# Kernel optimization log

Hardware: AMD Instinct MI355X
Metric: run time of the kernel (lower is better)

## Reference

```python
import jax, jax.numpy as jnp
import numpy as np

N, D, E = 50000, 128, 800000
BN_EPS = 1e-3  # keras BatchNormalization default


def _ffn_block(x, g, b, m, v, W, bias):
    # BatchNorm (inference) -> Dropout (identity at inference) -> Dense + exact GELU
    xn = (x - m) * g * jax.lax.rsqrt(v + BN_EPS) + b
    return jax.nn.gelu(xn @ W + bias, approximate=False)


def setup_inputs() -> dict:
    key = jax.random.key(0)
    ks = jax.random.split(key, 24)
    inp = {
        "node_reps": jax.random.normal(ks[0], (N, D), dtype=jnp.float32),
        "edges": jax.random.randint(ks[1], (2, E), 0, N, dtype=jnp.int32),
        "edge_weights": jax.random.uniform(ks[2], (E,), dtype=jnp.float32),
    }
    def bn(i, dim):
        return (jax.random.normal(ks[i], (dim,)) * 0.1 + 1.0,   # gamma
                jax.random.normal(ks[i + 1], (dim,)) * 0.1,      # beta
                jax.random.normal(ks[i + 2], (dim,)) * 0.1,      # moving mean
                jax.random.uniform(ks[i + 3], (dim,)) + 0.5)     # moving var (>0)
    # prepare FFN: two blocks, D->D then D->D
    inp["pre_bn1_g"], inp["pre_bn1_b"], inp["pre_bn1_m"], inp["pre_bn1_v"] = bn(3, D)
    inp["pre_w1"] = jax.random.normal(ks[7], (D, D)) * (1.0 / np.sqrt(D))
    inp["pre_b1"] = jnp.zeros((D,), jnp.float32)
    inp["pre_bn2_g"], inp["pre_bn2_b"], inp["pre_bn2_m"], inp["pre_bn2_v"] = bn(8, D)
    inp["pre_w2"] = jax.random.normal(ks[12], (D, D)) * (1.0 / np.sqrt(D))
    inp["pre_b2"] = jnp.zeros((D,), jnp.float32)
    # update FFN: concat -> 2D input, then D->D
    inp["upd_bn1_g"], inp["upd_bn1_b"], inp["upd_bn1_m"], inp["upd_bn1_v"] = bn(13, 2 * D)
    inp["upd_w1"] = jax.random.normal(ks[17], (2 * D, D)) * (1.0 / np.sqrt(2 * D))
    inp["upd_b1"] = jnp.zeros((D,), jnp.float32)
    inp["upd_bn2_g"], inp["upd_bn2_b"], inp["upd_bn2_m"], inp["upd_bn2_v"] = bn(18, D)
    inp["upd_w2"] = jax.random.normal(ks[22], (D, D)) * (1.0 / np.sqrt(D))
    inp["upd_b2"] = jnp.zeros((D,), jnp.float32)
    return inp


def reference(node_reps, edges, edge_weights,
              pre_bn1_g, pre_bn1_b, pre_bn1_m, pre_bn1_v, pre_w1, pre_b1,
              pre_bn2_g, pre_bn2_b, pre_bn2_m, pre_bn2_v, pre_w2, pre_b2,
              upd_bn1_g, upd_bn1_b, upd_bn1_m, upd_bn1_v, upd_w1, upd_b1,
              upd_bn2_g, upd_bn2_b, upd_bn2_m, upd_bn2_v, upd_w2, upd_b2):
    num_nodes = node_reps.shape[0]
    node_idx, nbr_idx = edges[0], edges[1]
    # gather neighbour representations [E, D]
    nbr = jnp.take(node_reps, nbr_idx, axis=0)
    # prepare: FFN then scale by edge weights
    msg = _ffn_block(nbr, pre_bn1_g, pre_bn1_b, pre_bn1_m, pre_bn1_v, pre_w1, pre_b1)
    msg = _ffn_block(msg, pre_bn2_g, pre_bn2_b, pre_bn2_m, pre_bn2_v, pre_w2, pre_b2)
    msg = msg * edge_weights[:, None]
    # aggregate: segment_sum scatter back to nodes [N, D]
    agg = jax.ops.segment_sum(msg, node_idx, num_segments=num_nodes)
    # update: concat + FFN, then L2 normalize
    h = jnp.concatenate([node_reps, agg], axis=-1)  # [N, 2D]
    out = _ffn_block(h, upd_bn1_g, upd_bn1_b, upd_bn1_m, upd_bn1_v, upd_w1, upd_b1)
    out = _ffn_block(out, upd_bn2_g, upd_bn2_b, upd_bn2_m, upd_bn2_v, upd_w2, upd_b2)
    out = out * jax.lax.rsqrt(jnp.maximum(jnp.sum(out * out, axis=-1, keepdims=True), 1e-12))
    return out
```

## Files before the change

### kernel.cpp

```cpp
#include <hip/hip_runtime.h>
#include <hip/hip_bf16.h>
#include <math.h>

#define NN 50000
#define DD 128
#define EE 800000

static constexpr float BN_EPS = 1e-3f;

typedef __attribute__((ext_vector_type(8))) short bf16x8;
typedef __attribute__((ext_vector_type(4))) float f32x4;

#define MFMA16(a, b, c) __builtin_amdgcn_mfma_f32_16x16x32_bf16((a), (b), (c), 0, 0, 0)

__device__ __forceinline__ float gelu_f(float x) {
    float ax = fabsf(x) * 0.7071067811865475f;
    float t = __builtin_amdgcn_rcpf(fmaf(0.3275911f, ax, 1.0f));
    float p = t * fmaf(t, fmaf(t, fmaf(t, fmaf(t, 1.061405429f, -1.453152027f),
                                       1.421413741f), -0.284496736f), 0.254829592f);
    float e = __expf(-ax * ax);
    float er = fmaf(-p, e, 1.0f);
    float s = copysignf(er, x);
    return 0.5f * x * (1.0f + s);
}

__device__ __forceinline__ ushort f2bf_rn(float f) {
    uint u = __float_as_uint(f);
    return (ushort)((u + 0x7FFFu + ((u >> 16) & 1u)) >> 16);
}
__device__ __forceinline__ float bf2f(ushort h) {
    return __uint_as_float(((uint)h) << 16);
}

__device__ __forceinline__ uint pk2(float a, float b) {
    __hip_bfloat162 t = __float22bfloat162_rn(make_float2(a, b));
    uint r;
    __builtin_memcpy(&r, &t, 4);
    return r;
}

__device__ __forceinline__ void cvt_hilo(float4 x0, float4 x1, bf16x8& h, bf16x8& l) {
    float f[8] = {x0.x, x0.y, x0.z, x0.w, x1.x, x1.y, x1.z, x1.w};
    union U { uint u[4]; bf16x8 v; } uh, ul;
    #pragma unroll
    for (int j = 0; j < 4; ++j) {
        uint p = pk2(f[2 * j], f[2 * j + 1]);
        uh.u[j] = p;
        float h0 = __uint_as_float(p << 16);
        float h1 = __uint_as_float(p & 0xFFFF0000u);
        ul.u[j] = pk2(f[2 * j] - h0, f[2 * j + 1] - h1);
    }
    h = uh.v;
    l = ul.v;
}

__device__ __forceinline__ void pack_one(const float* __restrict__ W, const float* __restrict__ g,
                                         const float* __restrict__ v, ushort* __restrict__ hi,
                                         ushort* __restrict__ lo, int K, int idx) {
    int k = idx >> 7, col = idx & 127;
    float s = g[k] * rsqrtf(v[k] + BN_EPS);
    float f = s * W[idx];
    int S = K >> 5;
    int st = k >> 5, gq = (k >> 3) & 3, j = k & 7;
    int c = col >> 4, ln = (gq << 4) | (col & 15);
    int o = ((c * S + st) * 64 + ln) * 8 + j;
    ushort hb = f2bf_rn(f);
    hi[o] = hb;
    lo[o] = f2bf_rn(f - bf2f(hb));
}

__global__ void pack_all(
    const float* __restrict__ w1, const float* __restrict__ g1, const float* __restrict__ v1,
    ushort* __restrict__ W1h, ushort* __restrict__ W1l,
    const float* __restrict__ w2, const float* __restrict__ g2, const float* __restrict__ v2,
    ushort* __restrict__ W2h, ushort* __restrict__ W2l,
    const float* __restrict__ u1, const float* __restrict__ g3, const float* __restrict__ v3,
    ushort* __restrict__ U1h, ushort* __restrict__ U1l,
    const float* __restrict__ u2, const float* __restrict__ g4, const float* __restrict__ v4,
    ushort* __restrict__ U2h, ushort* __restrict__ U2l)
{
    int idx = blockIdx.x * 256 + threadIdx.x;
    if (idx < 16384)       pack_one(w1, g1, v1, W1h, W1l, 128, idx);
    else if (idx < 32768)  pack_one(w2, g2, v2, W2h, W2l, 128, idx - 16384);
    else if (idx < 65536)  pack_one(u1, g3, v3, U1h, U1l, 256, idx - 32768);
    else                   pack_one(u2, g4, v4, U2h, U2l, 128, idx - 65536);
}

__global__ void init_bias(const float* __restrict__ b1, const float* __restrict__ b2,
                          const float* __restrict__ ub1, const float* __restrict__ ub2,
                          float* __restrict__ B1f, float* __restrict__ B2f,
                          float* __restrict__ C1f, float* __restrict__ C2f) {
    int t = threadIdx.x;
    B1f[t] = b1[t]; B2f[t] = b2[t]; C1f[t] = ub1[t]; C2f[t] = ub2[t];
}

__global__ __launch_bounds__(256) void fold_all(
    const float* __restrict__ w1, const float* __restrict__ g1, const float* __restrict__ b1,
    const float* __restrict__ m1, const float* __restrict__ v1, float* __restrict__ B1f,
    const float* __restrict__ w2, const float* __restrict__ g2, const float* __restrict__ b2,
    const float* __restrict__ m2, const float* __restrict__ v2, float* __restrict__ B2f,
    const float* __restrict__ u1, const float* __restrict__ g3, const float* __restrict__ b3,
    const float* __restrict__ m3, const float* __restrict__ v3, float* __restrict__ C1f,
    const float* __restrict__ u2, const float* __restrict__ g4, const float* __restrict__ b4,
    const float* __restrict__ m4, const float* __restrict__ v4, float* __restrict__ C2f,
    int* __restrict__ cnt, int* __restrict__ spillCnt)
{
    for (int i = blockIdx.x * 256 + threadIdx.x; i < NN + 1; i += 20 * 256) {
        if (i < NN) cnt[i] = 0; else spillCnt[0] = 0;
    }

    const int rs = blockIdx.x * 32;
    const float *W, *g, *bb, *m, *v;
    float* bf;
    int k0;
    if (rs < 128)      { W = w1; g = g1; bb = b1; m = m1; v = v1; bf = B1f; k0 = rs; }
    else if (rs < 256) { W = w2; g = g2; bb = b2; m = m2; v = v2; bf = B2f; k0 = rs - 128; }
    else if (rs < 512) { W = u1; g = g3; bb = b3; m = m3; v = v3; bf = C1f; k0 = rs - 256; }
    else               { W = u2; g = g4; bb = b4; m = m4; v = v4; bf = C2f; k0 = rs - 512; }

    const int t = threadIdx.x, j = t & 127, h = t >> 7;
    float acc = 0.f;
    #pragma unroll
    for (int kk = 0; kk < 16; ++kk) {
        int k = k0 + h * 16 + kk;
        float s = g[k] * rsqrtf(v[k] + BN_EPS);
        float tt = bb[k] - m[k] * s;
        acc = fmaf(tt, W[k * DD + j], acc);
    }
    __shared__ float S[256];
    S[t] = acc;
    __syncthreads();
    if (h == 0) atomicAdd(&bf[j], S[j] + S[128 + j]);
}

#define YLD 136
#define BCAP 56
#define SPILL_CAP 100000
#define NCHUNK 400
#define CHSZ (EE / NCHUNK)
#define PSZ 6250
#define FILLB (NCHUNK * 8)

__global__ __launch_bounds__(512, 4) void prep_fill(
    const float* __restrict__ reps, const int* __restrict__ edges,
    const ushort* __restrict__ W1h, const ushort* __restrict__ W1l, const float* __restrict__ B1,
    const ushort* __restrict__ W2h, const ushort* __restrict__ W2l, const float* __restrict__ B2,
    ushort* __restrict__ msgN,
    int* __restrict__ cnt, int* __restrict__ spillCnt,
    int* __restrict__ spill, int* __restrict__ bucket)
{
    __shared__ ushort Yh[128 * YLD];

    if (blockIdx.x < FILLB) {
        const int part = blockIdx.x & 7;
        const int ch   = blockIdx.x >> 3;
        const int lo = part * PSZ, hi2 = lo + PSZ;
        const int base = ch * CHSZ;
        for (int i = threadIdx.x; i < CHSZ; i += 512) {
            int e = base + i;
            int d = edges[e];
            if (d >= lo && d < hi2) {
                int s = atomicAdd(&cnt[d], 1);
                if (s < BCAP) bucket[d * BCAP + s] = e;
                else { int sl = atomicAdd(spillCnt, 1); if (sl < SPILL_CAP) spill[sl] = e; }
            }
        }
        return;
    }

    const int pb = blockIdx.x - FILLB;
    if (pb >= 391) return;
    const int t = threadIdx.x;
    const int w = t >> 6, l = t & 63, lg = l >> 4, lr = l & 15;
    const int n0 = pb * 128;
    int n = n0 + w * 16 + lr;
    int nc = n < NN ? n : NN - 1;
    const float* src = reps + (size_t)nc * DD;

    float b1v[8], b2v[8];
    #pragma unroll
    for (int c = 0; c < 8; ++c) { b1v[c] = B1[c * 16 + lr]; b2v[c] = B2[c * 16 + lr]; }

    f32x4 acc[8];
    #pragma unroll
    for (int c = 0; c < 8; ++c) acc[c] = (f32x4)(0.f);

    #pragma unroll
    for (int s = 0; s < 4; ++s) {
        float4 x0 = *reinterpret_cast<const float4*>(src + s * 32 + lg * 8);
        float4 x1 = *reinterpret_cast<const float4*>(src + s * 32 + lg * 8 + 4);
        bf16x8 ah, al;
        cvt_hilo(x0, x1, ah, al);
        #pragma unroll
        for (int c = 0; c < 8; ++c) {
            bf16x8 bh = *reinterpret_cast<const bf16x8*>(W1h + (size_t)((c * 4 + s) * 64 + l) * 8);
            bf16x8 bl = *reinterpret_cast<const bf16x8*>(W1l + (size_t)((c * 4 + s) * 64 + l) * 8);
            acc[c] = MFMA16(al, bh, acc[c]);
            acc[c] = MFMA16(ah, bl, acc[c]);
            acc[c] = MFMA16(ah, bh, acc[c]);
        }
    }
    #pragma unroll
    for (int c = 0; c < 8; ++c) {
        #pragma unroll
        for (int i = 0; i < 4; ++i) {
            float yv = gelu_f(acc[c][i] + b1v[c]);
            Yh[(w * 16 + lg * 4 + i) * YLD + c * 16 + lr] = f2bf_rn(yv);
        }
    }

    #pragma unroll
    for (int c = 0; c < 8; ++c) acc[c] = (f32x4)(0.f);
    const ushort* yr = Yh + (w * 16 + lr) * YLD;
    #pragma unroll
    for (int s = 0; s < 4; ++s) {
        bf16x8 ah = *reinterpret_cast<const bf16x8*>(yr + s * 32 + lg * 8);
        #pragma unroll
        for (int c = 0; c < 8; ++c) {
            bf16x8 bh = *reinterpret_cast<const bf16x8*>(W2h + (size_t)((c * 4 + s) * 64 + l) * 8);
            bf16x8 bl = *reinterpret_cast<const bf16x8*>(W2l + (size_t)((c * 4 + s) * 64 + l) * 8);
            acc[c] = MFMA16(ah, bl, acc[c]);
            acc[c] = MFMA16(ah, bh, acc[c]);
        }
    }

    const int nrow = n0 + w * 16 + lg * 4;
    #pragma unroll
    for (int i = 0; i < 4; ++i) {
        if (nrow + i < NN) {
            #pragma unroll
            for (int c = 0; c < 8; ++c)
                msgN[(size_t)(nrow + i) * DD + c * 16 + lr] = f2bf_rn(gelu_f(acc[c][i] + b2v[c]));
        }
    }
}

__global__ __launch_bounds__(256, 4) void agg_node(
    const float* __restrict__ reps, const int* __restrict__ edges, const float* __restrict__ ew,
    const int* __restrict__ bucket, const int* __restrict__ cnt,
    const int* __restrict__ spillCnt, const int* __restrict__ spill,
    const ushort* __restrict__ msgN,
    const ushort* __restrict__ U1h, const ushort* __restrict__ U1l, const float* __restrict__ C1,
    const ushort* __restrict__ U2h, const ushort* __restrict__ U2l, const float* __restrict__ C2,
    float* __restrict__ out)
{
    __shared__ ushort aggL[64 * YLD];
    __shared__ ushort Yh[64 * YLD];
    const int t = threadIdx.x;
    const int n0 = blockIdx.x * 64;

    {
        const int g = t >> 4, la = t & 15;
        const ushort* base = msgN + la * 8;
        for (int it = 0; it < 4; ++it) {
            const int nl = g * 4 + it;
            const int node = n0 + nl;
            float acc[8] = {0.f, 0.f, 0.f, 0.f, 0.f, 0.f, 0.f, 0.f};
            if (node < NN) {
                const int dc = cnt[node];
                const int deg = dc < BCAP ? dc : BCAP;
                const int* b = bucket + node * BCAP;
                int k = 0;
                for (; k + 3 < deg; k += 4) {
                    int e0 = b[k], e1 = b[k + 1], e2 = b[k + 2], e3 = b[k + 3];
                    int q0 = edges[EE + e0], q1 = edges[EE + e1];
                    int q2 = edges[EE + e2], q3 = edges[EE + e3];
                    float w0 = ew[e0], w1 = ew[e1], w2 = ew[e2], w3 = ew[e3];
                    bf16x8 m0 = *reinterpret_cast<const bf16x8*>(base + (size_t)q0 * DD);
                    bf16x8 m1 = *reinterpret_cast<const bf16x8*>(base + (size_t)q1 * DD);
                    bf16x8 m2 = *reinterpret_cast<const bf16x8*>(base + (size_t)q2 * DD);
                    bf16x8 m3 = *reinterpret_cast<const bf16x8*>(base + (size_t)q3 * DD);
                    #pragma unroll
                    for (int j = 0; j < 8; ++j) {
                        acc[j] = fmaf(w0, bf2f((ushort)m0[j]), acc[j]);
                        acc[j] = fmaf(w1, bf2f((ushort)m1[j]), acc[j]);
                        acc[j] = fmaf(w2, bf2f((ushort)m2[j]), acc[j]);
                        acc[j] = fmaf(w3, bf2f((ushort)m3[j]), acc[j]);
                    }
                }
                for (; k < deg; ++k) {
                    int e0 = b[k];
                    int q0 = edges[EE + e0];
                    float w0 = ew[e0];
                    bf16x8 m0 = *reinterpret_cast<const bf16x8*>(base + (size_t)q0 * DD);
                    #pragma unroll
                    for (int j = 0; j < 8; ++j) acc[j] = fmaf(w0, bf2f((ushort)m0[j]), acc[j]);
                }
                if (dc > BCAP) {
                    int sc = spillCnt[0]; if (sc > SPILL_CAP) sc = SPILL_CAP;
                    for (int i = 0; i < sc; ++i) {
                        int eid = spill[i];
                        if (edges[eid] == node) {
                            int q0 = edges[EE + eid];
                            float w0 = ew[eid];
                            bf16x8 m0 = *reinterpret_cast<const bf16x8*>(base + (size_t)q0 * DD);
                            #pragma unroll
                            for (int j = 0; j < 8; ++j)
                                acc[j] = fmaf(w0, bf2f((ushort)m0[j]), acc[j]);
                        }
                    }
                }
            }
            uint4 o;
            o.x = pk2(acc[0], acc[1]);
            o.y = pk2(acc[2], acc[3]);
            o.z = pk2(acc[4], acc[5]);
            o.w = pk2(acc[6], acc[7]);
            *reinterpret_cast<uint4*>(&aggL[nl * YLD + la * 8]) = o;
        }
    }
    __syncthreads();

    const int w = t >> 6, l = t & 63, lg = l >> 4, lr = l & 15;
    int n = n0 + w * 16 + lr;
    int nc = n < NN ? n : NN - 1;

    float c1v[8], c2v[8];
    #pragma unroll
    for (int c = 0; c < 8; ++c) { c1v[c] = C1[c * 16 + lr]; c2v[c] = C2[c * 16 + lr]; }

    f32x4 acc[8];
    #pragma unroll
    for (int c = 0; c < 8; ++c) acc[c] = (f32x4)(0.f);

    #pragma unroll
    for (int s = 0; s < 4; ++s) {
        const float* sp = reps + (size_t)nc * DD + s * 32 + lg * 8;
        float4 x0 = *reinterpret_cast<const float4*>(sp);
        float4 x1 = *reinterpret_cast<const float4*>(sp + 4);
        bf16x8 ah, al;
        cvt_hilo(x0, x1, ah, al);
        #pragma unroll
        for (int c = 0; c < 8; ++c) {
            bf16x8 bh = *reinterpret_cast<const bf16x8*>(U1h + (size_t)((c * 8 + s) * 64 + l) * 8);
            bf16x8 bl = *reinterpret_cast<const bf16x8*>(U1l + (size_t)((c * 8 + s) * 64 + l) * 8);
            acc[c] = MFMA16(al, bh, acc[c]);
            acc[c] = MFMA16(ah, bl, acc[c]);
            acc[c] = MFMA16(ah, bh, acc[c]);
        }
    }
    const ushort* ar = aggL + (w * 16 + lr) * YLD;
    #pragma unroll
    for (int s = 4; s < 8; ++s) {
        bf16x8 ah = *reinterpret_cast<const bf16x8*>(ar + (s - 4) * 32 + lg * 8);
        #pragma unroll
        for (int c = 0; c < 8; ++c) {
            bf16x8 bh = *reinterpret_cast<const bf16x8*>(U1h + (size_t)((c * 8 + s) * 64 + l) * 8);
            bf16x8 bl = *reinterpret_cast<const bf16x8*>(U1l + (size_t)((c * 8 + s) * 64 + l) * 8);
            acc[c] = MFMA16(ah, bl, acc[c]);
            acc[c] = MFMA16(ah, bh, acc[c]);
        }
    }
    #pragma unroll
    for (int c = 0; c < 8; ++c) {
        #pragma unroll
        for (int i = 0; i < 4; ++i) {
            float yv = gelu_f(acc[c][i] + c1v[c]);
            Yh[(w * 16 + lg * 4 + i) * YLD + c * 16 + lr] = f2bf_rn(yv);
        }
    }

    #pragma unroll
    for (int c = 0; c < 8; ++c) acc[c] = (f32x4)(0.f);
    const ushort* yr = Yh + (w * 16 + lr) * YLD;
    #pragma unroll
    for (int s = 0; s < 4; ++s) {
        bf16x8 ah = *reinterpret_cast<const bf16x8*>(yr + s * 32 + lg * 8);
        #pragma unroll
        for (int c = 0; c < 8; ++c) {
            bf16x8 bh = *reinterpret_cast<const bf16x8*>(U2h + (size_t)((c * 4 + s) * 64 + l) * 8);
            bf16x8 bl = *reinterpret_cast<const bf16x8*>(U2l + (size_t)((c * 4 + s) * 64 + l) * 8);
            acc[c] = MFMA16(ah, bl, acc[c]);
            acc[c] = MFMA16(ah, bh, acc[c]);
        }
    }

    float ssq[4] = {0.f, 0.f, 0.f, 0.f};
    #pragma unroll
    for (int c = 0; c < 8; ++c) {
        #pragma unroll
        for (int i = 0; i < 4; ++i) {
            float vv = gelu_f(acc[c][i] + c2v[c]);
            acc[c][i] = vv;
            ssq[i] = fmaf(vv, vv, ssq[i]);
        }
    }
    #pragma unroll
    for (int i = 0; i < 4; ++i) {
        #pragma unroll
        for (int msk = 1; msk < 16; msk <<= 1) ssq[i] += __shfl_xor(ssq[i], msk);
        ssq[i] = rsqrtf(fmaxf(ssq[i], 1e-12f));
    }
    const int nrow = n0 + w * 16 + lg * 4;
    #pragma unroll
    for (int i = 0; i < 4; ++i) {
        if (nrow + i < NN) {
            #pragma unroll
            for (int c = 0; c < 8; ++c)
                out[(size_t)(nrow + i) * DD + c * 16 + lr] = acc[c][i] * ssq[i];
        }
    }
}

extern "C" void kernel_launch(void* const* d_in, const int* in_sizes, int n_in,
                              void* d_out, int out_size, void* d_ws, size_t ws_size,
                              hipStream_t stream)
{
    const float* reps = (const float*)d_in[0];
    const int*   edges = (const int*)d_in[1];
    const float* ew   = (const float*)d_in[2];
    const float* bn1g = (const float*)d_in[3];
    const float* bn1b = (const float*)d_in[4];
    const float* bn1m = (const float*)d_in[5];
    const float* bn1v = (const float*)d_in[6];
    const float* w1   = (const float*)d_in[7];
    const float* b1   = (const float*)d_in[8];
    const float* bn2g = (const float*)d_in[9];
    const float* bn2b = (const float*)d_in[10];
    const float* bn2m = (const float*)d_in[11];
    const float* bn2v = (const float*)d_in[12];
    const float* w2   = (const float*)d_in[13];
    const float* b2   = (const float*)d_in[14];
    const float* ubn1g = (const float*)d_in[15];
    const float* ubn1b = (const float*)d_in[16];
    const float* ubn1m = (const float*)d_in[17];
    const float* ubn1v = (const float*)d_in[18];
    const float* u1    = (const float*)d_in[19];
    const float* ub1   = (const float*)d_in[20];
    const float* ubn2g = (const float*)d_in[21];
    const float* ubn2b = (const float*)d_in[22];
    const float* ubn2m = (const float*)d_in[23];
    const float* ubn2v = (const float*)d_in[24];
    const float* u2    = (const float*)d_in[25];
    const float* ub2   = (const float*)d_in[26];

    char* wsb = (char*)d_ws;
    ushort* msgN     = (ushort*)wsb;
    int*    bucket   = (int*)(wsb + 12800000);
    int*    cnt      = (int*)(wsb + 24000000);
    int*    spillCnt = (int*)(wsb + 24200000);
    int*    spill    = (int*)(wsb + 24200016);
    float*  B1f      = (float*)(wsb + 24600016);
    float*  B2f = B1f + 128;
    float*  C1f = B2f + 128;
    float*  C2f = C1f + 128;
    ushort* up  = (ushort*)(C2f + 128);
    ushort* W1h = up;
    ushort* W1l = W1h + 16384;
    ushort* W2h = W1l + 16384;
    ushort* W2l = W2h + 16384;
    ushort* U1h = W2l + 16384;
    ushort* U1l = U1h + 32768;
    ushort* U2h = U1l + 32768;
    ushort* U2l = U2h + 16384;
    if (ws_size < 24950000) return;

    init_bias<<<1, 128, 0, stream>>>(b1, b2, ub1, ub2, B1f, B2f, C1f, C2f);
    pack_all<<<320, 256, 0, stream>>>(w1, bn1g, bn1v, W1h, W1l,
                                      w2, bn2g, bn2v, W2h, W2l,
                                      u1, ubn1g, ubn1v, U1h, U1l,
                                      u2, ubn2g, ubn2v, U2h, U2l);
    fold_all<<<20, 256, 0, stream>>>(w1, bn1g, bn1b, bn1m, bn1v, B1f,
                                     w2, bn2g, bn2b, bn2m, bn2v, B2f,
                                     u1, ubn1g, ubn1b, ubn1m, ubn1v, C1f,
                                     u2, ubn2g, ubn2b, ubn2m, ubn2v, C2f,
                                     cnt, spillCnt);

    prep_fill<<<FILLB + 392, 512, 0, stream>>>(reps, edges, W1h, W1l, B1f,
                                               W2h, W2l, B2f, msgN,
                                               cnt, spillCnt, spill, bucket);
    agg_node<<<(NN + 63) / 64, 256, 0, stream>>>(reps, edges, ew, bucket, cnt,
                                                 spillCnt, spill, msgN,
                                                 U1h, U1l, C1f, U2h, U2l, C2f,
                                                 (float*)d_out);
}
```

Baseline: 163.2 us.

## Double agg_node block to 512 threads, splitting output columns across wave halves

agg_node now launches 512 threads per 64-node block. The gather phase handles two nodes per 16-lane group instead of four, and each wave computes half of the 128 output columns for its 16 rows. This means an extra barrier between the two update GEMMs, plus a shared-memory exchange of partial sums of squares for the L2 normalisation. The aim is more parallel gather latency hiding and fewer registers per thread, at the cost of added syncs and launch_bounds(512,8) register pressure limits.

After: 161.7 us. About the same (-0.9%).

```diff
diff --git a/kernel.cpp b/kernel.cpp
--- a/kernel.cpp
+++ b/kernel.cpp
@@ -235,7 +235,7 @@
     }
 }
 
-__global__ __launch_bounds__(256, 4) void agg_node(
+__global__ __launch_bounds__(512, 8) void agg_node(
     const float* __restrict__ reps, const int* __restrict__ edges, const float* __restrict__ ew,
     const int* __restrict__ bucket, const int* __restrict__ cnt,
     const int* __restrict__ spillCnt, const int* __restrict__ spill,
@@ -246,14 +246,16 @@
 {
     __shared__ ushort aggL[64 * YLD];
     __shared__ ushort Yh[64 * YLD];
+    __shared__ float ssqP[2][64];
     const int t = threadIdx.x;
     const int n0 = blockIdx.x * 64;
 
     {
         const int g = t >> 4, la = t & 15;
         const ushort* base = msgN + la * 8;
-        for (int it = 0; it < 4; ++it) {
-            const int nl = g * 4 + it;
+        #pragma unroll
+        for (int it = 0; it < 2; ++it) {
+            const int nl = g * 2 + it;
             const int node = n0 + nl;
             float acc[8] = {0.f, 0.f, 0.f, 0.f, 0.f, 0.f, 0.f, 0.f};
             if (node < NN) {
@@ -312,16 +314,20 @@
     __syncthreads();
 
     const int w = t >> 6, l = t & 63, lg = l >> 4, lr = l & 15;
-    int n = n0 + w * 16 + lr;
+    const int wr = w & 3, hh = w >> 2;
+    int n = n0 + wr * 16 + lr;
     int nc = n < NN ? n : NN - 1;
 
-    float c1v[8], c2v[8];
-    #pragma unroll
-    for (int c = 0; c < 8; ++c) { c1v[c] = C1[c * 16 + lr]; c2v[c] = C2[c * 16 + lr]; }
-
-    f32x4 acc[8];
-    #pragma unroll
-    for (int c = 0; c < 8; ++c) acc[c] = (f32x4)(0.f);
+    float c1v[4], c2v[4];
+    #pragma unroll
+    for (int cc = 0; cc < 4; ++cc) {
+        c1v[cc] = C1[(4 * hh + cc) * 16 + lr];
+        c2v[cc] = C2[(4 * hh + cc) * 16 + lr];
+    }
+
+    f32x4 acc[4];
+    #pragma unroll
+    for (int cc = 0; cc < 4; ++cc) acc[cc] = (f32x4)(0.f);
 
     #pragma unroll
     for (int s = 0; s < 4; ++s) {
@@ -331,57 +337,61 @@
         bf16x8 ah, al;
         cvt_hilo(x0, x1, ah, al);
         #pragma unroll
-        for (int c = 0; c < 8; ++c) {
+        for (int cc = 0; cc < 4; ++cc) {
+            int c = 4 * hh + cc;
             bf16x8 bh = *reinterpret_cast<const bf16x8*>(U1h + (size_t)((c * 8 + s) * 64 + l) * 8);
             bf16x8 bl = *reinterpret_cast<const bf16x8*>(U1l + (size_t)((c * 8 + s) * 64 + l) * 8);
-            acc[c] = MFMA16(al, bh, acc[c]);
-            acc[c] = MFMA16(ah, bl, acc[c]);
-            acc[c] = MFMA16(ah, bh, acc[c]);
-        }
-    }
-    const ushort* ar = aggL + (w * 16 + lr) * YLD;
+            acc[cc] = MFMA16(al, bh, acc[cc]);
+            acc[cc] = MFMA16(ah, bl, acc[cc]);
+            acc[cc] = MFMA16(ah, bh, acc[cc]);
+        }
+    }
+    const ushort* ar = aggL + (wr * 16 + lr) * YLD;
     #pragma unroll
     for (int s = 4; s < 8; ++s) {
         bf16x8 ah = *reinterpret_cast<const bf16x8*>(ar + (s - 4) * 32 + lg * 8);
         #pragma unroll
-        for (int c = 0; c < 8; ++c) {
+        for (int cc = 0; cc < 4; ++cc) {
+            int c = 4 * hh + cc;
             bf16x8 bh = *reinterpret_cast<const bf16x8*>(U1h + (size_t)((c * 8 + s) * 64 + l) * 8);
             bf16x8 bl = *reinterpret_cast<const bf16x8*>(U1l + (size_t)((c * 8 + s) * 64 + l) * 8);
-            acc[c] = MFMA16(ah, bl, acc[c]);
-            acc[c] = MFMA16(ah, bh, acc[c]);
-        }
-    }
-    #pragma unroll
-    for (int c = 0; c < 8; ++c) {
+            acc[cc] = MFMA16(ah, bl, acc[cc]);
+            acc[cc] = MFMA16(ah, bh, acc[cc]);
+        }
+    }
+    #pragma unroll
+    for (int cc = 0; cc < 4; ++cc) {
         #pragma unroll
         for (int i = 0; i < 4; ++i) {
-            float yv = gelu_f(acc[c][i] + c1v[c]);
-            Yh[(w * 16 + lg * 4 + i) * YLD + c * 16 + lr] = f2bf_rn(yv);
-        }
-    }
-
-    #pragma unroll
-    for (int c = 0; c < 8; ++c) acc[c] = (f32x4)(0.f);
-    const ushort* yr = Yh + (w * 16 + lr) * YLD;
+            float yv = gelu_f(acc[cc][i] + c1v[cc]);
+            Yh[(wr * 16 + lg * 4 + i) * YLD + (4 * hh + cc) * 16 + lr] = f2bf_rn(yv);
+        }
+    }
+    __syncthreads();
+
+    #pragma unroll
+    for (int cc = 0; cc < 4; ++cc) acc[cc] = (f32x4)(0.f);
+    const ushort* yr2 = Yh + (wr * 16 + lr) * YLD;
     #pragma unroll
     for (int s = 0; s < 4; ++s) {
-        bf16x8 ah = *reinterpret_cast<const bf16x8*>(yr + s * 32 + lg * 8);
-        #pragma unroll
-        for (int c = 0; c < 8; ++c) {
+        bf16x8 ah = *reinterpret_cast<const bf16x8*>(yr2 + s * 32 + lg * 8);
+        #pragma unroll
+        for (int cc = 0; cc < 4; ++cc) {
+            int c = 4 * hh + cc;
             bf16x8 bh = *reinterpret_cast<const bf16x8*>(U2h + (size_t)((c * 4 + s) * 64 + l) * 8);
             bf16x8 bl = *reinterpret_cast<const bf16x8*>(U2l + (size_t)((c * 4 + s) * 64 + l) * 8);
-            acc[c] = MFMA16(ah, bl, acc[c]);
-            acc[c] = MFMA16(ah, bh, acc[c]);
+            acc[cc] = MFMA16(ah, bl, acc[cc]);
+            acc[cc] = MFMA16(ah, bh, acc[cc]);
         }
     }
 
     float ssq[4] = {0.f, 0.f, 0.f, 0.f};
     #pragma unroll
-    for (int c = 0; c < 8; ++c) {
+    for (int cc = 0; cc < 4; ++cc) {
         #pragma unroll
         for (int i = 0; i < 4; ++i) {
-            float vv = gelu_f(acc[c][i] + c2v[c]);
-            acc[c][i] = vv;
+            float vv = gelu_f(acc[cc][i] + c2v[cc]);
+            acc[cc][i] = vv;
             ssq[i] = fmaf(vv, vv, ssq[i]);
         }
     }
@@ -389,15 +399,21 @@
     for (int i = 0; i < 4; ++i) {
         #pragma unroll
         for (int msk = 1; msk < 16; msk <<= 1) ssq[i] += __shfl_xor(ssq[i], msk);
-        ssq[i] = rsqrtf(fmaxf(ssq[i], 1e-12f));
-    }
-    const int nrow = n0 + w * 16 + lg * 4;
+    }
+    const int row0 = wr * 16 + lg * 4;
+    if (lr == 0) {
+        #pragma unroll
+        for (int i = 0; i < 4; ++i) ssqP[hh][row0 + i] = ssq[i];
+    }
+    __syncthreads();
     #pragma unroll
     for (int i = 0; i < 4; ++i) {
-        if (nrow + i < NN) {
+        float tot = ssqP[0][row0 + i] + ssqP[1][row0 + i];
+        float sc = rsqrtf(fmaxf(tot, 1e-12f));
+        if (n0 + row0 + i < NN) {
             #pragma unroll
-            for (int c = 0; c < 8; ++c)
-                out[(size_t)(nrow + i) * DD + c * 16 + lr] = acc[c][i] * ssq[i];
+            for (int cc = 0; cc < 4; ++cc)
+                out[(size_t)(n0 + row0 + i) * DD + (4 * hh + cc) * 16 + lr] = acc[cc][i] * sc;
         }
     }
 }
@@ -469,7 +485,7 @@
     prep_fill<<<FILLB + 392, 512, 0, stream>>>(reps, edges, W1h, W1l, B1f,
                                                W2h, W2l, B2f, msgN,
                                                cnt, spillCnt, spill, bucket);
-    agg_node<<<(NN + 63) / 64, 256, 0, stream>>>(reps, edges, ew, bucket, cnt,
+    agg_node<<<(NN + 63) / 64, 512, 0, stream>>>(reps, edges, ew, bucket, cnt,
                                                  spillCnt, spill, msgN,
                                                  U1h, U1l, C1f, U2h, U2l, C2f,
                                                  (float*)d_out);
```
